# Performance work log

Hardware: AMD Instinct MI355X
Metric: run time of the kernel (lower is better)

## Reference

```python
import jax, jax.numpy as jnp
import numpy as np

N_AST = 200000
N_TEST = 10000
H = 128
NUM_AST_LABELS = 128
AST_CONTENT = 256
NUM_CLASSES = 2
N_LAYERS = 5
E_AA, E_AT, E_TA = 2000000, 500000, 500000


def seg_mean(msg, dst, n):
    # mean aggregation of edge messages per destination node
    s = jax.ops.segment_sum(msg, dst, num_segments=n)
    d = jax.ops.segment_sum(jnp.ones((dst.shape[0], 1), msg.dtype), dst, num_segments=n)
    return s / jnp.maximum(d, 1.0)


def gcn_layer(h_ast, h_test, src_aa, dst_aa, src_at, dst_at, src_ta, dst_ta,
              W_aa, W_at, W_ta, b_ast, b_test):
    # transform-then-aggregate per canonical edge type, sum over edge types per dst ntype
    m_aa = seg_mean((h_ast @ W_aa)[src_aa], dst_aa, N_AST)
    m_ta = seg_mean((h_test @ W_ta)[src_ta], dst_ta, N_AST)
    new_ast = jax.nn.relu(m_aa + m_ta + b_ast)
    m_at = seg_mean((h_ast @ W_at)[src_at], dst_at, N_TEST)
    new_test = jax.nn.relu(m_at + b_test)
    return new_ast, new_test


def setup_inputs() -> dict:
    key = jax.random.key(0)
    ks = jax.random.split(key, 16)
    Hh = H // 2
    inp = {
        "ast_label": jax.random.randint(ks[0], (N_AST,), 0, NUM_AST_LABELS),
        "ast_content": jax.random.normal(ks[1], (N_AST, AST_CONTENT), jnp.float32),
        "src_aa": jax.random.randint(ks[2], (E_AA,), 0, N_AST, jnp.int32),
        "dst_aa": jax.random.randint(ks[3], (E_AA,), 0, N_AST, jnp.int32),
        "src_at": jax.random.randint(ks[4], (E_AT,), 0, N_AST, jnp.int32),
        "dst_at": jax.random.randint(ks[5], (E_AT,), 0, N_TEST, jnp.int32),
        "src_ta": jax.random.randint(ks[6], (E_TA,), 0, N_TEST, jnp.int32),
        "dst_ta": jax.random.randint(ks[7], (E_TA,), 0, N_AST, jnp.int32),
        "n_test": N_TEST,
        "ast_label_emb": jax.random.normal(ks[8], (NUM_AST_LABELS, Hh), jnp.float32) * 0.1,
        "ast_content_W": jax.random.normal(ks[9], (AST_CONTENT, Hh), jnp.float32) * (1.0 / np.sqrt(AST_CONTENT)),
        "ast_content_b": jax.random.normal(ks[10], (Hh,), jnp.float32) * 0.1,
        "test_embedding": jax.random.normal(ks[11], (H,), jnp.float32),
        "W_aa": jax.random.normal(ks[12], (N_LAYERS, H, H), jnp.float32) * (1.0 / np.sqrt(H)),
        "W_at": jax.random.normal(ks[13], (N_LAYERS, H, H), jnp.float32) * (1.0 / np.sqrt(H)),
        "W_ta": jax.random.normal(ks[14], (N_LAYERS, H, H), jnp.float32) * (1.0 / np.sqrt(H)),
        "b_ast": jnp.zeros((N_LAYERS, H), jnp.float32),
        "b_test": jnp.zeros((N_LAYERS, H), jnp.float32),
        "dec_W": jax.random.normal(ks[15], (H, NUM_CLASSES), jnp.float32) * (1.0 / np.sqrt(H)),
        "dec_b": jnp.zeros((NUM_CLASSES,), jnp.float32),
    }
    return inp


def reference(ast_label, ast_content, src_aa, dst_aa, src_at, dst_at, src_ta, dst_ta,
              n_test, ast_label_emb, ast_content_W, ast_content_b, test_embedding,
              W_aa, W_at, W_ta, b_ast, b_test, dec_W, dec_b):
    # hetero node encoding: ast = [embedding(label) || linear(content)], test = broadcast learned vector
    h_ast = jnp.concatenate(
        [ast_label_emb[ast_label], ast_content @ ast_content_W + ast_content_b], axis=-1)
    h_test = jnp.broadcast_to(test_embedding[None, :], (n_test, H))

    def layer(i, ha, ht):
        return gcn_layer(ha, ht, src_aa, dst_aa, src_at, dst_at, src_ta, dst_ta,
                         W_aa[i], W_at[i], W_ta[i], b_ast[i], b_test[i])

    h_ast, h_test = layer(0, h_ast, h_test)
    res_a, res_t = h_ast, h_test
    h_ast, h_test = layer(1, h_ast, h_test)
    h_ast, h_test = res_a + h_ast, res_t + h_test
    h_ast, h_test = layer(2, h_ast, h_test)
    res_a, res_t = h_ast, h_test
    h_ast, h_test = layer(3, h_ast, h_test)
    h_ast, h_test = res_a + h_ast, res_t + h_test
    h_ast, h_test = layer(4, h_ast, h_test)

    logits = h_ast @ dec_W + dec_b  # ast_decode_node_func with num_classes>1 -> softmax
    pred = jax.nn.softmax(logits, axis=1)
    return logits, pred
```

## Files before the change

### kernel.cpp

```cpp
#include <hip/hip_runtime.h>

#define N_ASTN 200000
#define N_TESTN 10000
#define HDIM 128
#define E_AA_N 2000000
#define E_AT_N 500000
#define E_TA_N 500000

typedef __bf16 bf16x8 __attribute__((ext_vector_type(8)));
typedef float f32x4 __attribute__((ext_vector_type(4)));
typedef float f32x2 __attribute__((ext_vector_type(2)));

static __device__ __forceinline__ float bflo(unsigned u) {
    union { unsigned x; float f; } c; c.x = u << 16; return c.f;
}
static __device__ __forceinline__ float bfhi(unsigned u) {
    union { unsigned x; float f; } c; c.x = u & 0xffff0000u; return c.f;
}
static __device__ __forceinline__ unsigned short f2bf(float f) {
    union { float f; unsigned u; } c; c.f = f;
    unsigned u = c.u;
    return (unsigned short)((u + 0x7fffu + ((u >> 16) & 1u)) >> 16);
}
static __device__ __forceinline__ unsigned pack2(float a, float b) {
    return (unsigned)f2bf(a) | ((unsigned)f2bf(b) << 16);
}
static __device__ __forceinline__ f32x2 unpk(unsigned u) {
    union { unsigned q[2]; f32x2 v; } t;
    t.q[0] = u << 16;
    t.q[1] = u & 0xffff0000u;
    return t.v;
}


__global__ void detect_k(const unsigned short* __restrict__ p, int* __restrict__ flag) {
    __shared__ int cnt;
    if (threadIdx.x == 0) cnt = 0;
    __syncthreads();
    int local = 0;
    for (int i = threadIdx.x; i < 8192; i += 256) {
        unsigned e = ((unsigned)p[i] >> 7) & 0xFFu;
        if (e >= 158u) local++;
    }
    atomicAdd(&cnt, local);
    __syncthreads();
    if (threadIdx.x == 0) *flag = (cnt > 64) ? 1 : 0;
}


struct ConvSpec {
    const void* src[11];
    int off[11];
    int total;
};

__global__ void conv_params_k(ConvSpec spec, const int* __restrict__ flag,
                              unsigned short* __restrict__ dst) {
    int f32 = *flag;
    int i = blockIdx.x * blockDim.x + threadIdx.x;
    int stride = gridDim.x * blockDim.x;
    for (; i < spec.total; i += stride) {
        int s = 10;
        for (int k = 1; k < 11; k++) {
            if (i < spec.off[k]) { s = k - 1; break; }
        }
        int j = i - spec.off[s];
        unsigned short v;
        if (f32) v = f2bf(((const float*)spec.src[s])[j]);
        else     v = ((const unsigned short*)spec.src[s])[j];
        dst[i] = v;
    }
}


__global__ void count_k(const int* __restrict__ dst, int nE, int nNode,
                        int* __restrict__ cnt) {
    int i = blockIdx.x * blockDim.x + threadIdx.x;
    int stride = gridDim.x * blockDim.x;
    for (; i < nE; i += stride) {
        unsigned d = (unsigned)dst[i];
        if (d < (unsigned)nNode) atomicAdd(&cnt[d], 1);
    }
}

__global__ void scan_bsum(const int* __restrict__ in, int n, int* __restrict__ bsum) {
    __shared__ int lds[256];
    int b = blockIdx.x, tid = threadIdx.x;
    int base = b * 1024 + tid * 4;
    int s = 0;
#pragma unroll
    for (int j = 0; j < 4; j++) { int i = base + j; if (i < n) s += in[i]; }
    lds[tid] = s; __syncthreads();
    for (int off = 128; off; off >>= 1) {
        if (tid < off) lds[tid] += lds[tid + off];
        __syncthreads();
    }
    if (tid == 0) bsum[b] = lds[0];
}

__global__ void scan_top(int* __restrict__ bsum, int nb) {
    __shared__ int lds[256];
    int tid = threadIdx.x;
    int v = (tid < nb) ? bsum[tid] : 0;
    lds[tid] = v; __syncthreads();
    for (int off = 1; off < 256; off <<= 1) {
        int t = (tid >= off) ? lds[tid - off] : 0;
        __syncthreads();
        lds[tid] += t;
        __syncthreads();
    }
    if (tid < nb) bsum[tid] = lds[tid] - v;
}

__global__ void scan_final(const int* __restrict__ in, int n,
                           const int* __restrict__ bsum, int* __restrict__ out) {
    __shared__ int lds[256];
    int b = blockIdx.x, tid = threadIdx.x;
    int base = b * 1024 + tid * 4;
    int v[4]; int s = 0;
#pragma unroll
    for (int j = 0; j < 4; j++) { int i = base + j; v[j] = (i < n) ? in[i] : 0; s += v[j]; }
    lds[tid] = s; __syncthreads();
    for (int off = 1; off < 256; off <<= 1) {
        int t = (tid >= off) ? lds[tid - off] : 0;
        __syncthreads();
        lds[tid] += t;
        __syncthreads();
    }
    int texcl = lds[tid] - s;
    int run = bsum[b] + texcl;
#pragma unroll
    for (int j = 0; j < 4; j++) { int i = base + j; if (i < n) out[i] = run; run += v[j]; }
}

__global__ void fill_k(const int* __restrict__ src, const int* __restrict__ dst, int nE,
                       int nNode, const int* __restrict__ indptr, int* __restrict__ cursor,
                       int* __restrict__ edges) {
    int i = blockIdx.x * blockDim.x + threadIdx.x;
    int stride = gridDim.x * blockDim.x;
    for (; i < nE; i += stride) {
        unsigned d = (unsigned)dst[i];
        if (d >= (unsigned)nNode) continue;
        unsigned pos = (unsigned)(indptr[d] + atomicAdd(&cursor[d], 1));
        if (pos < (unsigned)nE) edges[pos] = src[i];
    }
}


__global__ void encode_emb(const int* __restrict__ label, const unsigned* __restrict__ embU,
                           unsigned* __restrict__ hAU) {
    int idx = blockIdx.x * blockDim.x + threadIdx.x;
    int node = idx >> 5, c = idx & 31;
    int lb = label[node] & 127;
    hAU[node * 64 + c] = embU[lb * 32 + c];
}

__global__ void init_test(const unsigned* __restrict__ tEmbU, unsigned* __restrict__ hTU) {
    int idx = blockIdx.x * blockDim.x + threadIdx.x;
    int node = idx >> 6, c = idx & 63;
    hTU[node * 64 + c] = tEmbU[c];
}


template<int NST>
__global__ void __launch_bounds__(256) gemm_rowblk(
    const void* __restrict__ Araw, const __bf16* __restrict__ W,
    const __bf16* __restrict__ bias, __bf16* __restrict__ C,
    int M, int K, int lda, int ldc, const int* __restrict__ flagp)
{
    __shared__ __bf16 sW[16384];
    int a_f32 = flagp ? *flagp : 0;
    int tid = threadIdx.x;
    int nkb = K >> 5;
    const int N = NST * 16;
    int ngroups = nkb * NST * 64;
    for (int g = tid; g < ngroups; g += 256) {
        int l = g & 63;
        int sk = g >> 6;
        int s = sk % NST, kb = sk / NST;
        int krow = kb * 32 + ((l >> 4) << 3);
        int col = s * 16 + (l & 15);
        bf16x8 tmp;
#pragma unroll
        for (int j = 0; j < 8; j++) tmp[j] = W[(krow + j) * N + col];
        *(bf16x8*)(&sW[g * 8]) = tmp;
    }
    __syncthreads();
    int wave = tid >> 6, lane = tid & 63;
    int mrow = lane & 15, koff = (lane >> 4) << 3;
    int tilesM = M >> 4;
    for (int mt = blockIdx.x * 4 + wave; mt < tilesM; mt += gridDim.x * 4) {
        int m0 = mt << 4;
        f32x4 acc[NST];
#pragma unroll
        for (int s = 0; s < NST; s++) acc[s] = (f32x4){0.f, 0.f, 0.f, 0.f};
        for (int kb = 0; kb < nkb; kb++) {
            bf16x8 a;
            if (a_f32) {
                const float* Af = (const float*)Araw + (size_t)(m0 + mrow) * lda + koff + kb * 32;
                f32x4 x0 = *(const f32x4*)Af;
                f32x4 x1 = *(const f32x4*)(Af + 4);
#pragma unroll
                for (int j = 0; j < 4; j++) { a[j] = (__bf16)x0[j]; a[4 + j] = (__bf16)x1[j]; }
            } else {
                const __bf16* Ab = (const __bf16*)Araw + (size_t)(m0 + mrow) * lda + koff + kb * 32;
                a = *(const bf16x8*)Ab;
            }
#pragma unroll
            for (int s = 0; s < NST; s++) {
                bf16x8 b = *(const bf16x8*)(&sW[((kb * NST + s) * 64 + lane) * 8]);
                acc[s] = __builtin_amdgcn_mfma_f32_16x16x32_bf16(a, b, acc[s], 0, 0, 0);
            }
        }
        int r0 = m0 + ((lane >> 4) << 2);
#pragma unroll
        for (int s = 0; s < NST; s++) {
            int col = s * 16 + (lane & 15);
            float bv = bias ? (float)bias[col] : 0.f;
#pragma unroll
            for (int i = 0; i < 4; i++)
                C[(size_t)(r0 + i) * ldc + col] = (__bf16)(acc[s][i] + bv);
        }
    }
}


__global__ void __launch_bounds__(256) test_transform(
    const __bf16* __restrict__ A, const __bf16* __restrict__ W,
    const __bf16* __restrict__ bias, __bf16* __restrict__ C,
    int M, int resflag)
{
    __shared__ __bf16 sW[16384];
    int tid = threadIdx.x;
    for (int g = tid; g < 2048; g += 256) {
        int l = g & 63;
        int sk = g >> 6;
        int s = sk & 7, kb = sk >> 3;
        int krow = kb * 32 + ((l >> 4) << 3);
        int col = s * 16 + (l & 15);
        bf16x8 tmp;
#pragma unroll
        for (int j = 0; j < 8; j++) tmp[j] = W[(krow + j) * 128 + col];
        *(bf16x8*)(&sW[g * 8]) = tmp;
    }
    __syncthreads();
    int wave = tid >> 6, lane = tid & 63;
    int mrow = lane & 15, koff = (lane >> 4) << 3;
    int total = (M >> 4) * 8;
    for (int t = blockIdx.x * 4 + wave; t < total; t += gridDim.x * 4) {
        int s = t & 7;
        int m0 = (t >> 3) << 4;
        f32x4 acc = {0.f, 0.f, 0.f, 0.f};
#pragma unroll
        for (int kb = 0; kb < 4; kb++) {
            bf16x8 a = *(const bf16x8*)(A + (size_t)(m0 + mrow) * 128 + koff + kb * 32);
            bf16x8 b = *(const bf16x8*)(&sW[((kb * 8 + s) * 64 + lane) * 8]);
            acc = __builtin_amdgcn_mfma_f32_16x16x32_bf16(a, b, acc, 0, 0, 0);
        }
        int col = s * 16 + (lane & 15);
        float bv = (float)bias[col];
        int r0 = m0 + ((lane >> 4) << 2);
#pragma unroll
        for (int i = 0; i < 4; i++) {
            float v = fmaxf(acc[i] + bv, 0.f);
            if (resflag) v += (float)C[(size_t)(r0 + i) * 128 + col];
            C[(size_t)(r0 + i) * 128 + col] = (__bf16)v;
        }
    }
}


__global__ void __launch_bounds__(256) ast_update(
    const uint4* __restrict__ TAq, const uint4* __restrict__ TTq,
    const int* __restrict__ ipA, const int* __restrict__ eA,
    const int* __restrict__ ipT, const int* __restrict__ eT,
    const uint4* __restrict__ biasq, unsigned* __restrict__ h,
    int n, int resflag)
{
    int wid = (blockIdx.x * blockDim.x + threadIdx.x) >> 6;
    int lane = threadIdx.x & 63;
    if (wid >= n) return;
    int g = lane >> 4, l = lane & 15;
    const char* TAb = (const char*)TAq;
    const char* TTb = (const char*)TTq;
    unsigned loff = (unsigned)l << 4;

    f32x2 sa[4] = {{0.f,0.f},{0.f,0.f},{0.f,0.f},{0.f,0.f}};
    int a0 = ipA[wid], a1 = ipA[wid + 1];
    {
        int e = a0 + g;
        for (; e + 4 < a1; e += 8) {
            unsigned o0 = ((unsigned)eA[e] << 8) + loff;
            unsigned o1 = ((unsigned)eA[e + 4] << 8) + loff;
            uint4 u0 = *(const uint4*)(TAb + o0);
            uint4 u1 = *(const uint4*)(TAb + o1);
            sa[0] += unpk(u0.x); sa[1] += unpk(u0.y);
            sa[2] += unpk(u0.z); sa[3] += unpk(u0.w);
            sa[0] += unpk(u1.x); sa[1] += unpk(u1.y);
            sa[2] += unpk(u1.z); sa[3] += unpk(u1.w);
        }
        if (e < a1) {
            unsigned o0 = ((unsigned)eA[e] << 8) + loff;
            uint4 u0 = *(const uint4*)(TAb + o0);
            sa[0] += unpk(u0.x); sa[1] += unpk(u0.y);
            sa[2] += unpk(u0.z); sa[3] += unpk(u0.w);
        }
    }
    f32x2 st[4] = {{0.f,0.f},{0.f,0.f},{0.f,0.f},{0.f,0.f}};
    int t0 = ipT[wid], t1 = ipT[wid + 1];
    {
        int e = t0 + g;
        for (; e + 4 < t1; e += 8) {
            unsigned o0 = ((unsigned)eT[e] << 8) + loff;
            unsigned o1 = ((unsigned)eT[e + 4] << 8) + loff;
            uint4 u0 = *(const uint4*)(TTb + o0);
            uint4 u1 = *(const uint4*)(TTb + o1);
            st[0] += unpk(u0.x); st[1] += unpk(u0.y);
            st[2] += unpk(u0.z); st[3] += unpk(u0.w);
            st[0] += unpk(u1.x); st[1] += unpk(u1.y);
            st[2] += unpk(u1.z); st[3] += unpk(u1.w);
        }
        if (e < t1) {
            unsigned o0 = ((unsigned)eT[e] << 8) + loff;
            uint4 u0 = *(const uint4*)(TTb + o0);
            st[0] += unpk(u0.x); st[1] += unpk(u0.y);
            st[2] += unpk(u0.z); st[3] += unpk(u0.w);
        }
    }
#pragma unroll
    for (int j = 0; j < 4; j++) {
        sa[j].x += __shfl_xor(sa[j].x, 16);
        sa[j].y += __shfl_xor(sa[j].y, 16);
        sa[j].x += __shfl_xor(sa[j].x, 32);
        sa[j].y += __shfl_xor(sa[j].y, 32);
        st[j].x += __shfl_xor(st[j].x, 16);
        st[j].y += __shfl_xor(st[j].y, 16);
        st[j].x += __shfl_xor(st[j].x, 32);
        st[j].y += __shfl_xor(st[j].y, 32);
    }
    if (g == 0) {
        int da = a1 - a0; if (da < 1) da = 1;
        int dt = t1 - t0; if (dt < 1) dt = 1;
        float inva = 1.0f / (float)da, invt = 1.0f / (float)dt;
        uint4 ub = biasq[l];
        float v[8];
        v[0] = sa[0].x * inva + st[0].x * invt + bflo(ub.x);
        v[1] = sa[0].y * inva + st[0].y * invt + bfhi(ub.x);
        v[2] = sa[1].x * inva + st[1].x * invt + bflo(ub.y);
        v[3] = sa[1].y * inva + st[1].y * invt + bfhi(ub.y);
        v[4] = sa[2].x * inva + st[2].x * invt + bflo(ub.z);
        v[5] = sa[2].y * inva + st[2].y * invt + bfhi(ub.z);
        v[6] = sa[3].x * inva + st[3].x * invt + bflo(ub.w);
        v[7] = sa[3].y * inva + st[3].y * invt + bfhi(ub.w);
#pragma unroll
        for (int j = 0; j < 8; j++) v[j] = fmaxf(v[j], 0.f);
        uint4* hq = (uint4*)h;
        if (resflag) {
            uint4 r = hq[(size_t)wid * 16 + l];
            v[0] += bflo(r.x); v[1] += bfhi(r.x);
            v[2] += bflo(r.y); v[3] += bfhi(r.y);
            v[4] += bflo(r.z); v[5] += bfhi(r.z);
            v[6] += bflo(r.w); v[7] += bfhi(r.w);
        }
        uint4 o;
        o.x = pack2(v[0], v[1]); o.y = pack2(v[2], v[3]);
        o.z = pack2(v[4], v[5]); o.w = pack2(v[6], v[7]);
        hq[(size_t)wid * 16 + l] = o;
    }
}


__global__ void __launch_bounds__(256) agg_at_k(
    const uint4* __restrict__ Hq,
    const int* __restrict__ ip, const int* __restrict__ ed,
    uint4* __restrict__ outq, int n)
{
    int wid = (blockIdx.x * blockDim.x + threadIdx.x) >> 6;
    int lane = threadIdx.x & 63;
    if (wid >= n) return;
    int g = lane >> 4, l = lane & 15;
    const char* Hb = (const char*)Hq;
    unsigned loff = (unsigned)l << 4;
    f32x2 sa[4] = {{0.f,0.f},{0.f,0.f},{0.f,0.f},{0.f,0.f}};
    int a0 = ip[wid], a1 = ip[wid + 1];
    {
        int e = a0 + g;
        for (; e + 4 < a1; e += 8) {
            unsigned o0 = ((unsigned)ed[e] << 8) + loff;
            unsigned o1 = ((unsigned)ed[e + 4] << 8) + loff;
            uint4 u0 = *(const uint4*)(Hb + o0);
            uint4 u1 = *(const uint4*)(Hb + o1);
            sa[0] += unpk(u0.x); sa[1] += unpk(u0.y);
            sa[2] += unpk(u0.z); sa[3] += unpk(u0.w);
            sa[0] += unpk(u1.x); sa[1] += unpk(u1.y);
            sa[2] += unpk(u1.z); sa[3] += unpk(u1.w);
        }
        if (e < a1) {
            unsigned o0 = ((unsigned)ed[e] << 8) + loff;
            uint4 u0 = *(const uint4*)(Hb + o0);
            sa[0] += unpk(u0.x); sa[1] += unpk(u0.y);
            sa[2] += unpk(u0.z); sa[3] += unpk(u0.w);
        }
    }
#pragma unroll
    for (int j = 0; j < 4; j++) {
        sa[j].x += __shfl_xor(sa[j].x, 16);
        sa[j].y += __shfl_xor(sa[j].y, 16);
        sa[j].x += __shfl_xor(sa[j].x, 32);
        sa[j].y += __shfl_xor(sa[j].y, 32);
    }
    if (g == 0) {
        int da = a1 - a0; if (da < 1) da = 1;
        float inv = 1.0f / (float)da;
        uint4 o;
        o.x = pack2(sa[0].x * inv, sa[0].y * inv);
        o.y = pack2(sa[1].x * inv, sa[1].y * inv);
        o.z = pack2(sa[2].x * inv, sa[2].y * inv);
        o.w = pack2(sa[3].x * inv, sa[3].y * inv);
        outq[(size_t)wid * 16 + l] = o;
    }
}


__global__ void __launch_bounds__(256) decoder_k(
    const unsigned* __restrict__ h, const unsigned* __restrict__ wU,
    const unsigned* __restrict__ decbU, void* __restrict__ out, int n,
    const int* __restrict__ flagp)
{
    int f32out = *flagp;
    int wid = (blockIdx.x * blockDim.x + threadIdx.x) >> 6;
    int lane = threadIdx.x & 63;
    if (wid >= n) return;
    unsigned u = h[(size_t)wid * 64 + lane];
    float h0 = bflo(u), h1 = bfhi(u);
    unsigned w0 = wU[lane * 2], w1 = wU[lane * 2 + 1];
    float p0 = h0 * bflo(w0) + h1 * bflo(w1);
    float p1 = h0 * bfhi(w0) + h1 * bfhi(w1);
    for (int off = 32; off; off >>= 1) {
        p0 += __shfl_down(p0, off);
        p1 += __shfl_down(p1, off);
    }
    if (lane == 0) {
        unsigned db = decbU[0];
        float l0 = p0 + bflo(db);
        float l1 = p1 + bfhi(db);
        float m = fmaxf(l0, l1);
        float e0 = __expf(l0 - m), e1 = __expf(l1 - m);
        float invs = 1.0f / (e0 + e1);
        if (f32out) {
            float* o = (float*)out;
            o[wid * 2 + 0] = l0;
            o[wid * 2 + 1] = l1;
            o[2 * N_ASTN + wid * 2 + 0] = e0 * invs;
            o[2 * N_ASTN + wid * 2 + 1] = e1 * invs;
        } else {
            unsigned short* o = (unsigned short*)out;
            o[wid * 2 + 0] = f2bf(l0);
            o[wid * 2 + 1] = f2bf(l1);
            o[2 * N_ASTN + wid * 2 + 0] = f2bf(e0 * invs);
            o[2 * N_ASTN + wid * 2 + 1] = f2bf(e1 * invs);
        }
    }
}


extern "C" void kernel_launch(void* const* d_in, const int* in_sizes, int n_in,
                              void* d_out, int out_size, void* d_ws, size_t ws_size,
                              hipStream_t stream) {
    const int* ast_label = (const int*)d_in[0];
    const void* ast_content = d_in[1];
    const int* src_aa = (const int*)d_in[2];
    const int* dst_aa = (const int*)d_in[3];
    const int* src_at = (const int*)d_in[4];
    const int* dst_at = (const int*)d_in[5];
    const int* src_ta = (const int*)d_in[6];
    const int* dst_ta = (const int*)d_in[7];

    char* ws = (char*)d_ws;
    size_t off = 0;
    auto alloc = [&](size_t bytes) {
        char* p = ws + off;
        off += (bytes + 255) & ~(size_t)255;
        return p;
    };
    int* flag = (int*)alloc(256);
    const int P_EMB = 0, P_CW = 8192, P_CB = 24576, P_TEMB = 24640, P_WAA = 24768,
              P_WAT = 106688, P_WTA = 188608, P_BAST = 270528, P_BTEST = 271168,
              P_DECW = 271808, P_DECB = 272064, P_TOTAL = 272066;
    __bf16* params = (__bf16*)alloc((size_t)P_TOTAL * 2);
    __bf16* hA = (__bf16*)alloc((size_t)N_ASTN * HDIM * 2);
    __bf16* TA = (__bf16*)alloc((size_t)N_ASTN * HDIM * 2);
    __bf16* hT = (__bf16*)alloc((size_t)N_TESTN * HDIM * 2);
    __bf16* TT = (__bf16*)alloc((size_t)N_TESTN * HDIM * 2);
    int* ip_aa = (int*)alloc((size_t)(N_ASTN + 1) * 4);
    int* ip_ta = (int*)alloc((size_t)(N_ASTN + 1) * 4);
    int* ip_at = (int*)alloc((size_t)(N_TESTN + 1) * 4);
    int* e_aa = (int*)alloc((size_t)E_AA_N * 4);
    int* e_ta = (int*)alloc((size_t)E_TA_N * 4);
    int* e_at = (int*)alloc((size_t)E_AT_N * 4);
    char* zbase = alloc(((size_t)(N_ASTN + 1 + N_ASTN) * 2 + (N_TESTN + 1 + N_TESTN)) * 4);
    int* cnt_aa = (int*)zbase;
    int* cur_aa = cnt_aa + (N_ASTN + 1);
    int* cnt_ta = cur_aa + N_ASTN;
    int* cur_ta = cnt_ta + (N_ASTN + 1);
    int* cnt_at = cur_ta + N_ASTN;
    int* cur_at = cnt_at + (N_TESTN + 1);
    size_t zbytes = ((size_t)(N_ASTN + 1 + N_ASTN) * 2 + (N_TESTN + 1 + N_TESTN)) * 4;
    int* bsumA = (int*)alloc(256 * 4);
    int* bsumT = (int*)alloc(256 * 4);
    int* bsumX = (int*)alloc(256 * 4);
    __bf16* aggAT = (__bf16*)zbase;

    if (ws_size < off) {
        hipMemsetAsync(d_out, 0, (size_t)out_size * 2, stream);
        return;
    }

    detect_k<<<1, 256, 0, stream>>>((const unsigned short*)ast_content, flag);
    ConvSpec spec;
    spec.src[0] = d_in[9];  spec.off[0] = P_EMB;
    spec.src[1] = d_in[10]; spec.off[1] = P_CW;
    spec.src[2] = d_in[11]; spec.off[2] = P_CB;
    spec.src[3] = d_in[12]; spec.off[3] = P_TEMB;
    spec.src[4] = d_in[13]; spec.off[4] = P_WAA;
    spec.src[5] = d_in[14]; spec.off[5] = P_WAT;
    spec.src[6] = d_in[15]; spec.off[6] = P_WTA;
    spec.src[7] = d_in[16]; spec.off[7] = P_BAST;
    spec.src[8] = d_in[17]; spec.off[8] = P_BTEST;
    spec.src[9] = d_in[18]; spec.off[9] = P_DECW;
    spec.src[10] = d_in[19]; spec.off[10] = P_DECB;
    spec.total = P_TOTAL;
    conv_params_k<<<256, 256, 0, stream>>>(spec, flag, (unsigned short*)params);

    hipMemsetAsync(zbase, 0, zbytes, stream);

    count_k<<<4096, 256, 0, stream>>>(dst_aa, E_AA_N, N_ASTN, cnt_aa);
    count_k<<<2048, 256, 0, stream>>>(dst_ta, E_TA_N, N_ASTN, cnt_ta);
    count_k<<<2048, 256, 0, stream>>>(dst_at, E_AT_N, N_TESTN, cnt_at);

    const int nA = N_ASTN + 1, nT = N_TESTN + 1;
    const int nbA = (nA + 1023) / 1024, nbT = (nT + 1023) / 1024;
    scan_bsum<<<nbA, 256, 0, stream>>>(cnt_aa, nA, bsumA);
    scan_top<<<1, 256, 0, stream>>>(bsumA, nbA);
    scan_final<<<nbA, 256, 0, stream>>>(cnt_aa, nA, bsumA, ip_aa);
    scan_bsum<<<nbA, 256, 0, stream>>>(cnt_ta, nA, bsumT);
    scan_top<<<1, 256, 0, stream>>>(bsumT, nbA);
    scan_final<<<nbA, 256, 0, stream>>>(cnt_ta, nA, bsumT, ip_ta);
    scan_bsum<<<nbT, 256, 0, stream>>>(cnt_at, nT, bsumX);
    scan_top<<<1, 256, 0, stream>>>(bsumX, nbT);
    scan_final<<<nbT, 256, 0, stream>>>(cnt_at, nT, bsumX, ip_at);

    fill_k<<<4096, 256, 0, stream>>>(src_aa, dst_aa, E_AA_N, N_ASTN, ip_aa, cur_aa, e_aa);
    fill_k<<<2048, 256, 0, stream>>>(src_ta, dst_ta, E_TA_N, N_ASTN, ip_ta, cur_ta, e_ta);
    fill_k<<<2048, 256, 0, stream>>>(src_at, dst_at, E_AT_N, N_TESTN, ip_at, cur_at, e_at);

    encode_emb<<<N_ASTN * 32 / 256, 256, 0, stream>>>(ast_label, (const unsigned*)(params + P_EMB),
                                                      (unsigned*)hA);
    gemm_rowblk<4><<<1568, 256, 0, stream>>>(ast_content, params + P_CW, params + P_CB,
                                             hA + 64, N_ASTN, 256, 256, HDIM, flag);
    init_test<<<N_TESTN * 64 / 256, 256, 0, stream>>>((const unsigned*)(params + P_TEMB),
                                                      (unsigned*)hT);

    const int resflags[5] = {0, 1, 0, 1, 0};
    for (int l = 0; l < 5; l++) {
        const __bf16* Waa = params + P_WAA + (size_t)l * HDIM * HDIM;
        const __bf16* Wat = params + P_WAT + (size_t)l * HDIM * HDIM;
        const __bf16* Wta = params + P_WTA + (size_t)l * HDIM * HDIM;
        gemm_rowblk<8><<<160, 256, 0, stream>>>(hT, Wta, nullptr, TT, N_TESTN, HDIM, HDIM, HDIM, nullptr);
        agg_at_k<<<N_TESTN / 4, 256, 0, stream>>>(
            (const uint4*)hA, ip_at, e_at, (uint4*)aggAT, N_TESTN);
        gemm_rowblk<8><<<1568, 256, 0, stream>>>(hA, Waa, nullptr, TA, N_ASTN, HDIM, HDIM, HDIM, nullptr);
        test_transform<<<256, 256, 0, stream>>>(
            aggAT, Wat, params + P_BTEST + (size_t)l * HDIM, hT, N_TESTN, resflags[l]);
        ast_update<<<N_ASTN / 4, 256, 0, stream>>>(
            (const uint4*)TA, (const uint4*)TT, ip_aa, e_aa, ip_ta, e_ta,
            (const uint4*)(params + P_BAST + (size_t)l * HDIM), (unsigned*)hA,
            N_ASTN, resflags[l]);
    }

    decoder_k<<<N_ASTN / 4, 256, 0, stream>>>((const unsigned*)hA,
                                              (const unsigned*)(params + P_DECW),
                                              (const unsigned*)(params + P_DECB),
                                              d_out, N_ASTN, flag);
}
```

Baseline: 1.704 ms.

## Map one 16-lane group per node in gather-aggregation kernels

The two CSR gather kernels (ast_update and agg_at_k) now give each destination node a 16-lane group instead of a full 64-lane wavefront, so each wavefront handles four nodes. Each group walks that node's edges serially, two at a time. This drops the cross-group shuffle reduction and the idle lanes in the epilogue, and cuts the launched block count by four. In exchange, per-node memory-level parallelism is lower and nodes with different degrees in the same wavefront cause divergence.

```diff
diff --git a/kernel.cpp b/kernel.cpp
--- a/kernel.cpp
+++ b/kernel.cpp
@@ -277,21 +277,20 @@
     const uint4* __restrict__ biasq, unsigned* __restrict__ h,
     int n, int resflag)
 {
-    int wid = (blockIdx.x * blockDim.x + threadIdx.x) >> 6;
-    int lane = threadIdx.x & 63;
-    if (wid >= n) return;
-    int g = lane >> 4, l = lane & 15;
+    int node = (blockIdx.x * blockDim.x + threadIdx.x) >> 4;
+    int l = threadIdx.x & 15;
+    if (node >= n) return;
     const char* TAb = (const char*)TAq;
     const char* TTb = (const char*)TTq;
     unsigned loff = (unsigned)l << 4;
 
     f32x2 sa[4] = {{0.f,0.f},{0.f,0.f},{0.f,0.f},{0.f,0.f}};
-    int a0 = ipA[wid], a1 = ipA[wid + 1];
+    int a0 = ipA[node], a1 = ipA[node + 1];
     {
-        int e = a0 + g;
-        for (; e + 4 < a1; e += 8) {
+        int e = a0;
+        for (; e + 1 < a1; e += 2) {
             unsigned o0 = ((unsigned)eA[e] << 8) + loff;
-            unsigned o1 = ((unsigned)eA[e + 4] << 8) + loff;
+            unsigned o1 = ((unsigned)eA[e + 1] << 8) + loff;
             uint4 u0 = *(const uint4*)(TAb + o0);
             uint4 u1 = *(const uint4*)(TAb + o1);
             sa[0] += unpk(u0.x); sa[1] += unpk(u0.y);
@@ -307,12 +306,12 @@
         }
     }
     f32x2 st[4] = {{0.f,0.f},{0.f,0.f},{0.f,0.f},{0.f,0.f}};
-    int t0 = ipT[wid], t1 = ipT[wid + 1];
+    int t0 = ipT[node], t1 = ipT[node + 1];
     {
-        int e = t0 + g;
-        for (; e + 4 < t1; e += 8) {
+        int e = t0;
+        for (; e + 1 < t1; e += 2) {
             unsigned o0 = ((unsigned)eT[e] << 8) + loff;
-            unsigned o1 = ((unsigned)eT[e + 4] << 8) + loff;
+            unsigned o1 = ((unsigned)eT[e + 1] << 8) + loff;
             uint4 u0 = *(const uint4*)(TTb + o0);
             uint4 u1 = *(const uint4*)(TTb + o1);
             st[0] += unpk(u0.x); st[1] += unpk(u0.y);
@@ -327,46 +326,33 @@
             st[2] += unpk(u0.z); st[3] += unpk(u0.w);
         }
     }
-#pragma unroll
-    for (int j = 0; j < 4; j++) {
-        sa[j].x += __shfl_xor(sa[j].x, 16);
-        sa[j].y += __shfl_xor(sa[j].y, 16);
-        sa[j].x += __shfl_xor(sa[j].x, 32);
-        sa[j].y += __shfl_xor(sa[j].y, 32);
-        st[j].x += __shfl_xor(st[j].x, 16);
-        st[j].y += __shfl_xor(st[j].y, 16);
-        st[j].x += __shfl_xor(st[j].x, 32);
-        st[j].y += __shfl_xor(st[j].y, 32);
-    }
-    if (g == 0) {
-        int da = a1 - a0; if (da < 1) da = 1;
-        int dt = t1 - t0; if (dt < 1) dt = 1;
-        float inva = 1.0f / (float)da, invt = 1.0f / (float)dt;
-        uint4 ub = biasq[l];
-        float v[8];
-        v[0] = sa[0].x * inva + st[0].x * invt + bflo(ub.x);
-        v[1] = sa[0].y * inva + st[0].y * invt + bfhi(ub.x);
-        v[2] = sa[1].x * inva + st[1].x * invt + bflo(ub.y);
-        v[3] = sa[1].y * inva + st[1].y * invt + bfhi(ub.y);
-        v[4] = sa[2].x * inva + st[2].x * invt + bflo(ub.z);
-        v[5] = sa[2].y * inva + st[2].y * invt + bfhi(ub.z);
-        v[6] = sa[3].x * inva + st[3].x * invt + bflo(ub.w);
-        v[7] = sa[3].y * inva + st[3].y * invt + bfhi(ub.w);
-#pragma unroll
-        for (int j = 0; j < 8; j++) v[j] = fmaxf(v[j], 0.f);
-        uint4* hq = (uint4*)h;
-        if (resflag) {
-            uint4 r = hq[(size_t)wid * 16 + l];
-            v[0] += bflo(r.x); v[1] += bfhi(r.x);
-            v[2] += bflo(r.y); v[3] += bfhi(r.y);
-            v[4] += bflo(r.z); v[5] += bfhi(r.z);
-            v[6] += bflo(r.w); v[7] += bfhi(r.w);
-        }
-        uint4 o;
-        o.x = pack2(v[0], v[1]); o.y = pack2(v[2], v[3]);
-        o.z = pack2(v[4], v[5]); o.w = pack2(v[6], v[7]);
-        hq[(size_t)wid * 16 + l] = o;
-    }
+    int da = a1 - a0; if (da < 1) da = 1;
+    int dt = t1 - t0; if (dt < 1) dt = 1;
+    float inva = 1.0f / (float)da, invt = 1.0f / (float)dt;
+    uint4 ub = biasq[l];
+    float v[8];
+    v[0] = sa[0].x * inva + st[0].x * invt + bflo(ub.x);
+    v[1] = sa[0].y * inva + st[0].y * invt + bfhi(ub.x);
+    v[2] = sa[1].x * inva + st[1].x * invt + bflo(ub.y);
+    v[3] = sa[1].y * inva + st[1].y * invt + bfhi(ub.y);
+    v[4] = sa[2].x * inva + st[2].x * invt + bflo(ub.z);
+    v[5] = sa[2].y * inva + st[2].y * invt + bfhi(ub.z);
+    v[6] = sa[3].x * inva + st[3].x * invt + bflo(ub.w);
+    v[7] = sa[3].y * inva + st[3].y * invt + bfhi(ub.w);
+#pragma unroll
+    for (int j = 0; j < 8; j++) v[j] = fmaxf(v[j], 0.f);
+    uint4* hq = (uint4*)h;
+    if (resflag) {
+        uint4 r = hq[(size_t)node * 16 + l];
+        v[0] += bflo(r.x); v[1] += bfhi(r.x);
+        v[2] += bflo(r.y); v[3] += bfhi(r.y);
+        v[4] += bflo(r.z); v[5] += bfhi(r.z);
+        v[6] += bflo(r.w); v[7] += bfhi(r.w);
+    }
+    uint4 o;
+    o.x = pack2(v[0], v[1]); o.y = pack2(v[2], v[3]);
+    o.z = pack2(v[4], v[5]); o.w = pack2(v[6], v[7]);
+    hq[(size_t)node * 16 + l] = o;
 }
 
 
@@ -375,19 +361,18 @@
     const int* __restrict__ ip, const int* __restrict__ ed,
     uint4* __restrict__ outq, int n)
 {
-    int wid = (blockIdx.x * blockDim.x + threadIdx.x) >> 6;
-    int lane = threadIdx.x & 63;
-    if (wid >= n) return;
-    int g = lane >> 4, l = lane & 15;
+    int node = (blockIdx.x * blockDim.x + threadIdx.x) >> 4;
+    int l = threadIdx.x & 15;
+    if (node >= n) return;
     const char* Hb = (const char*)Hq;
     unsigned loff = (unsigned)l << 4;
     f32x2 sa[4] = {{0.f,0.f},{0.f,0.f},{0.f,0.f},{0.f,0.f}};
-    int a0 = ip[wid], a1 = ip[wid + 1];
+    int a0 = ip[node], a1 = ip[node + 1];
     {
-        int e = a0 + g;
-        for (; e + 4 < a1; e += 8) {
+        int e = a0;
+        for (; e + 1 < a1; e += 2) {
             unsigned o0 = ((unsigned)ed[e] << 8) + loff;
-            unsigned o1 = ((unsigned)ed[e + 4] << 8) + loff;
+            unsigned o1 = ((unsigned)ed[e + 1] << 8) + loff;
             uint4 u0 = *(const uint4*)(Hb + o0);
             uint4 u1 = *(const uint4*)(Hb + o1);
             sa[0] += unpk(u0.x); sa[1] += unpk(u0.y);
@@ -402,23 +387,14 @@
             sa[2] += unpk(u0.z); sa[3] += unpk(u0.w);
         }
     }
-#pragma unroll
-    for (int j = 0; j < 4; j++) {
-        sa[j].x += __shfl_xor(sa[j].x, 16);
-        sa[j].y += __shfl_xor(sa[j].y, 16);
-        sa[j].x += __shfl_xor(sa[j].x, 32);
-        sa[j].y += __shfl_xor(sa[j].y, 32);
-    }
-    if (g == 0) {
-        int da = a1 - a0; if (da < 1) da = 1;
-        float inv = 1.0f / (float)da;
-        uint4 o;
-        o.x = pack2(sa[0].x * inv, sa[0].y * inv);
-        o.y = pack2(sa[1].x * inv, sa[1].y * inv);
-        o.z = pack2(sa[2].x * inv, sa[2].y * inv);
-        o.w = pack2(sa[3].x * inv, sa[3].y * inv);
-        outq[(size_t)wid * 16 + l] = o;
-    }
+    int da = a1 - a0; if (da < 1) da = 1;
+    float inv = 1.0f / (float)da;
+    uint4 o;
+    o.x = pack2(sa[0].x * inv, sa[0].y * inv);
+    o.y = pack2(sa[1].x * inv, sa[1].y * inv);
+    o.z = pack2(sa[2].x * inv, sa[2].y * inv);
+    o.w = pack2(sa[3].x * inv, sa[3].y * inv);
+    outq[(size_t)node * 16 + l] = o;
 }
 
 
@@ -567,12 +543,12 @@
         const __bf16* Wat = params + P_WAT + (size_t)l * HDIM * HDIM;
         const __bf16* Wta = params + P_WTA + (size_t)l * HDIM * HDIM;
         gemm_rowblk<8><<<160, 256, 0, stream>>>(hT, Wta, nullptr, TT, N_TESTN, HDIM, HDIM, HDIM, nullptr);
-        agg_at_k<<<N_TESTN / 4, 256, 0, stream>>>(
+        agg_at_k<<<N_TESTN / 16, 256, 0, stream>>>(
             (const uint4*)hA, ip_at, e_at, (uint4*)aggAT, N_TESTN);
         gemm_rowblk<8><<<1568, 256, 0, stream>>>(hA, Waa, nullptr, TA, N_ASTN, HDIM, HDIM, HDIM, nullptr);
         test_transform<<<256, 256, 0, stream>>>(
             aggAT, Wat, params + P_BTEST + (size_t)l * HDIM, hT, N_TESTN, resflags[l]);
-        ast_update<<<N_ASTN / 4, 256, 0, stream>>>(
+        ast_update<<<N_ASTN / 16, 256, 0, stream>>>(
             (const uint4*)TA, (const uint4*)TT, ip_aa, e_aa, ip_ta, e_ta,
             (const uint4*)(params + P_BAST + (size_t)l * HDIM), (unsigned*)hA,
             N_ASTN, resflags[l]);
```

Measured after the change: 1.616 ms. 1.05x faster.
